# Optimization experiments

Hardware: AMD Instinct MI355X
Metric: run time of the kernel (lower is better)

The kernel has to match this reference:

```python
import jax, jax.numpy as jnp
import numpy as np

B, E, H, T = 32768, 64, 128, 12  # batch, embedding_dim, decoder_h_dim, pred_len


def setup_inputs() -> dict:
    key = jax.random.key(0)
    ks = jax.random.split(key, 13)
    f = lambda k, shape: jax.random.normal(k, shape, dtype=jnp.float32) * 0.05
    return {
        "last_pos": f(ks[0], (B, 2)),
        "last_pos_rel": f(ks[1], (B, 2)),
        "h0": f(ks[2], (1, B, H)),
        "c0": f(ks[3], (1, B, H)),
        "pred_ped_speed": jax.random.uniform(ks[4], (T, B, 1), dtype=jnp.float32),
        # spatial_embedding: Linear(3, E)
        "W_se": f(ks[5], (E, 3)),
        "b_se": f(ks[6], (E,)),
        # single-layer LSTM(E -> H), torch gate order [i, f, g, o]
        "W_ih": f(ks[7], (4 * H, E)),
        "W_hh": f(ks[8], (4 * H, H)),
        "b_ih": f(ks[9], (4 * H,)),
        "b_hh": f(ks[10], (4 * H,)),
        # hidden2pos: Linear(H, 2)
        "W_hp": f(ks[11], (2, H)),
        "b_hp": f(ks[12], (2,)),
    }


def reference(last_pos, last_pos_rel, h0, c0, pred_ped_speed,
              W_se, b_se, W_ih, W_hh, b_ih, b_hh, W_hp, b_hp):
    # train_or_test == 0 path: speed comes straight from pred_ped_speed
    Tlen = pred_ped_speed.shape[0]
    b_lstm = b_ih + b_hh
    # initial decoder input: embed concat([last_pos_rel, speed_0])  -> [B, E]
    x0 = jnp.concatenate([last_pos_rel, pred_ped_speed[0]], axis=1) @ W_se.T + b_se

    def step(carry, t):
        h, c, x, lp = carry  # h,c: [B,H]; x: [B,E]; lp: [B,2]
        gates = x @ W_ih.T + h @ W_hh.T + b_lstm           # [B, 4H]
        i, f_, g, o = jnp.split(gates, 4, axis=1)
        c = jax.nn.sigmoid(f_) * c + jax.nn.sigmoid(i) * jnp.tanh(g)
        h = jax.nn.sigmoid(o) * jnp.tanh(c)
        rel = h @ W_hp.T + b_hp                            # [B, 2]
        lp = rel + lp                                      # curr_pos -> last_pos
        # speed for next step; at final step torch keeps the previous speed
        spd = pred_ped_speed[jnp.minimum(t + 1, Tlen - 1)]
        x = jnp.concatenate([rel, spd], axis=1) @ W_se.T + b_se
        return (h, c, x, lp), rel

    (h, c, _, _), rels = jax.lax.scan(
        step, (h0[0], c0[0], x0, last_pos), jnp.arange(Tlen))
    # pred_traj_fake_rel: [T, B, 2]; final hidden state: [1, B, H]
    return rels, h[None]
```

## Files before the change

kernel.cpp:

```cpp
#include <hip/hip_runtime.h>

#define T_LEN 12
#define B_N   32768
#define H_N   128
#define E_N   64
#define BM    32

typedef __attribute__((ext_vector_type(8))) __bf16 bf16x8;
typedef __attribute__((ext_vector_type(8))) short  short8v;
typedef __attribute__((ext_vector_type(4))) float  f32x4;

__device__ __forceinline__ unsigned short f2bf(float f) {
  unsigned int u = __builtin_bit_cast(unsigned int, f);
  u += 0x7fffu + ((u >> 16) & 1u);
  return (unsigned short)(u >> 16);
}
__device__ __forceinline__ float sigm(float x) {
  return __builtin_amdgcn_rcpf(1.f + __builtin_amdgcn_exp2f(-1.4426950408889634f * x));
}
__device__ __forceinline__ float tanh_(float x) {
  return 1.f - 2.f * __builtin_amdgcn_rcpf(__builtin_amdgcn_exp2f(2.8853900817779268f * x) + 1.f);
}

__global__ void prep_kernel(const float* __restrict__ Wih, const float* __restrict__ Whh,
                            const float* __restrict__ bih, const float* __restrict__ bhh,
                            const float* __restrict__ Wse, const float* __restrict__ bse,
                            const float* __restrict__ Whp, const float* __restrict__ bhp,
                            unsigned short* __restrict__ Wf, float* __restrict__ u,
                            float* __restrict__ w0, float* __restrict__ G) {
  int i = blockIdx.x * 256 + threadIdx.x;
  if (i < 512 * 128) {
    int n = i >> 7, k = i & 127;
    float s = Whh[n * 128 + k];
    float wh0 = Whp[k], wh1 = Whp[128 + k];
    for (int e = 0; e < 64; ++e)
      s += Wih[n * 64 + e] * (Wse[e * 3 + 0] * wh0 + Wse[e * 3 + 1] * wh1);
    Wf[i] = f2bf(s);
  } else if (i < 512 * 128 + 2048) {
    int j = i - 512 * 128;
    int n = j >> 2, which = j & 3;
    float s = 0.f;
    if (which < 2) {
      for (int e = 0; e < 64; ++e) s += Wih[n * 64 + e] * Wse[e * 3 + which];
      G[n * 2 + which] = s;
    } else if (which == 2) {
      for (int e = 0; e < 64; ++e) s += Wih[n * 64 + e] * Wse[e * 3 + 2];
      u[n] = s;
    } else {
      for (int e = 0; e < 64; ++e)
        s += Wih[n * 64 + e] * (bse[e] + Wse[e * 3 + 0] * bhp[0] + Wse[e * 3 + 1] * bhp[1]);
      w0[n] = bih[n] + bhh[n] + s;
    }
  }
}

__launch_bounds__(512, 4)
__global__ void decoder_kernel(const float* __restrict__ lpr,
                               const float* __restrict__ h0,
                               const float* __restrict__ c0,
                               const float* __restrict__ pps,
                               const float* __restrict__ Whp,
                               const float* __restrict__ bhp,
                               const unsigned short* __restrict__ Wf,
                               const float* __restrict__ u,
                               const float* __restrict__ w0,
                               const float* __restrict__ G,
                               float* __restrict__ out_rel,
                               float* __restrict__ out_h) {
  __shared__ unsigned short WfL[256 * 128];
  __shared__ unsigned short hS[BM * 128];
  __shared__ unsigned short whpB[4 * 64 * 8];
  __shared__ float spdbuf[BM];
  __shared__ float dbuf[BM * 2];

  const int tid  = threadIdx.x;
  const int w    = tid >> 6;
  const int l    = tid & 63;
  const int l15  = l & 15;
  const int lg   = l >> 4;
  const int brow = blockIdx.x * BM;
  const int nh   = w * 16 + l15;
  const int swz  = (l15 & 7) << 4;
  char* hB  = (char*)hS;
  char* wB  = (char*)WfL;
  char* pB  = (char*)whpB;

  for (int i = tid; i < 256 * 16; i += 512) {
    int row = i >> 4, k16 = i & 15;
    short8v v = *(const short8v*)(Wf + (256 + row) * 128 + k16 * 8);
    int byte = (row * 256 + k16 * 16) ^ ((row & 7) << 4);
    *(short8v*)(wB + byte) = v;
  }
  short8v bw[2][4];
#pragma unroll
  for (int g = 0; g < 2; ++g)
#pragma unroll
    for (int ks = 0; ks < 4; ++ks)
      bw[g][ks] = *(const short8v*)(Wf + (g * 128 + nh) * 128 + ks * 32 + lg * 8);

  float ur[4], w0r[4];
#pragma unroll
  for (int g = 0; g < 4; ++g) { ur[g] = u[g * 128 + nh]; w0r[g] = w0[g * 128 + nh]; }

  f32x4 cst[2];
#pragma unroll
  for (int mt = 0; mt < 2; ++mt)
#pragma unroll
    for (int r = 0; r < 4; ++r)
      cst[mt][r] = c0[(brow + mt * 16 + lg * 4 + r) * H_N + nh];

  {
    int row = tid >> 4, k0 = (tid & 15) * 8;
    const float* src = h0 + (brow + row) * H_N + k0;
    unsigned short tmp[8];
#pragma unroll
    for (int j = 0; j < 8; ++j) tmp[j] = f2bf(src[j]);
    int byte = (row * 256 + k0 * 2) ^ ((row & 7) << 4);
    *(short8v*)(hB + byte) = *(short8v*)tmp;
  }
  if (tid < 256) {
    int ks = tid >> 6, ll = tid & 63, c = ll & 15, kg = ll >> 4;
    unsigned short tmp[8];
#pragma unroll
    for (int j = 0; j < 8; ++j)
      tmp[j] = (c < 2) ? f2bf(Whp[c * 128 + ks * 32 + kg * 8 + j]) : (unsigned short)0;
    *(short8v*)(pB + (ks * 64 + ll) * 16) = *(short8v*)tmp;
  }
  {
    int dot = tid >> 3, part = tid & 7;
    int row = dot >> 1, j = dot & 1;
    float s = 0.f;
    const float* hrow = h0 + (brow + row) * H_N + part * 16;
    const float* wrow = Whp + j * 128 + part * 16;
#pragma unroll
    for (int k = 0; k < 16; ++k) s += hrow[k] * wrow[k];
    s += __shfl_xor(s, 1); s += __shfl_xor(s, 2); s += __shfl_xor(s, 4);
    if (part == 0) dbuf[dot] = lpr[(brow + row) * 2 + j] - bhp[j] - s;
  }
  const float bhpr = (l15 < 2) ? bhp[l15] : 0.f;

#pragma unroll 1
  for (int t = 0; t < T_LEN; ++t) {
    __syncthreads();

    if (tid < BM) spdbuf[tid] = pps[t * B_N + brow + tid];

    f32x4 acc[4][2];
#pragma unroll
    for (int g = 0; g < 4; ++g)
#pragma unroll
      for (int mt = 0; mt < 2; ++mt) acc[g][mt] = (f32x4){0.f, 0.f, 0.f, 0.f};
    f32x4 relC = (f32x4){0.f, 0.f, 0.f, 0.f};

#pragma unroll
    for (int ks = 0; ks < 4; ++ks) {
      int kb = ks * 64 + lg * 16;
      bf16x8 a0 = __builtin_bit_cast(bf16x8, *(short8v*)(hB + ((l15 * 256 + kb) ^ swz)));
      bf16x8 a1 = __builtin_bit_cast(bf16x8, *(short8v*)(hB + (((16 + l15) * 256 + kb) ^ swz)));
      bf16x8 b2 = __builtin_bit_cast(bf16x8, *(short8v*)(wB + ((nh * 256 + kb) ^ swz)));
      bf16x8 b3 = __builtin_bit_cast(bf16x8, *(short8v*)(wB + 32768 + ((nh * 256 + kb) ^ swz)));
      acc[0][0] = __builtin_amdgcn_mfma_f32_16x16x32_bf16(a0, __builtin_bit_cast(bf16x8, bw[0][ks]), acc[0][0], 0, 0, 0);
      acc[0][1] = __builtin_amdgcn_mfma_f32_16x16x32_bf16(a1, __builtin_bit_cast(bf16x8, bw[0][ks]), acc[0][1], 0, 0, 0);
      acc[1][0] = __builtin_amdgcn_mfma_f32_16x16x32_bf16(a0, __builtin_bit_cast(bf16x8, bw[1][ks]), acc[1][0], 0, 0, 0);
      acc[1][1] = __builtin_amdgcn_mfma_f32_16x16x32_bf16(a1, __builtin_bit_cast(bf16x8, bw[1][ks]), acc[1][1], 0, 0, 0);
      acc[2][0] = __builtin_amdgcn_mfma_f32_16x16x32_bf16(a0, b2, acc[2][0], 0, 0, 0);
      acc[2][1] = __builtin_amdgcn_mfma_f32_16x16x32_bf16(a1, b2, acc[2][1], 0, 0, 0);
      acc[3][0] = __builtin_amdgcn_mfma_f32_16x16x32_bf16(a0, b3, acc[3][0], 0, 0, 0);
      acc[3][1] = __builtin_amdgcn_mfma_f32_16x16x32_bf16(a1, b3, acc[3][1], 0, 0, 0);
      if (w < 2 && t > 0) {
        bf16x8 wb = __builtin_bit_cast(bf16x8, *(short8v*)(pB + ks * 1024 + l * 16));
        relC = __builtin_amdgcn_mfma_f32_16x16x32_bf16(w == 0 ? a0 : a1, wb, relC, 0, 0, 0);
      }
    }
    if (w < 2 && t > 0 && l15 < 2) {
#pragma unroll
      for (int r = 0; r < 4; ++r)
        out_rel[(size_t)(t - 1) * B_N * 2 + (brow + w * 16 + lg * 4 + r) * 2 + l15] = relC[r] + bhpr;
    }

    __syncthreads();

#pragma unroll
    for (int mt = 0; mt < 2; ++mt) {
#pragma unroll
      for (int r = 0; r < 4; ++r) {
        int row = mt * 16 + lg * 4 + r;
        float spd = spdbuf[row];
        float gi = acc[0][mt][r] + w0r[0] + spd * ur[0];
        float gf = acc[1][mt][r] + w0r[1] + spd * ur[1];
        float gg = acc[2][mt][r] + w0r[2] + spd * ur[2];
        float go = acc[3][mt][r] + w0r[3] + spd * ur[3];
        if (t == 0) {
          float d0 = dbuf[row * 2 + 0], d1 = dbuf[row * 2 + 1];
          gi += d0 * G[(0 * 128 + nh) * 2 + 0] + d1 * G[(0 * 128 + nh) * 2 + 1];
          gf += d0 * G[(1 * 128 + nh) * 2 + 0] + d1 * G[(1 * 128 + nh) * 2 + 1];
          gg += d0 * G[(2 * 128 + nh) * 2 + 0] + d1 * G[(2 * 128 + nh) * 2 + 1];
          go += d0 * G[(3 * 128 + nh) * 2 + 0] + d1 * G[(3 * 128 + nh) * 2 + 1];
        }
        float cn = sigm(gf) * cst[mt][r] + sigm(gi) * tanh_(gg);
        cst[mt][r] = cn;
        float h = sigm(go) * tanh_(cn);
        hS[((row * 256 + nh * 2) ^ ((row & 7) << 4)) >> 1] = f2bf(h);
        if (t == T_LEN - 1) out_h[(brow + row) * H_N + nh] = h;
      }
    }
  }

  __syncthreads();
  if (w < 2) {
    f32x4 relC = (f32x4){0.f, 0.f, 0.f, 0.f};
#pragma unroll
    for (int ks = 0; ks < 4; ++ks) {
      int kb = ks * 64 + lg * 16;
      bf16x8 a = __builtin_bit_cast(bf16x8,
          *(short8v*)(hB + (((w * 16 + l15) * 256 + kb) ^ swz)));
      bf16x8 wb = __builtin_bit_cast(bf16x8, *(short8v*)(pB + ks * 1024 + l * 16));
      relC = __builtin_amdgcn_mfma_f32_16x16x32_bf16(a, wb, relC, 0, 0, 0);
    }
    if (l15 < 2) {
#pragma unroll
      for (int r = 0; r < 4; ++r)
        out_rel[(size_t)(T_LEN - 1) * B_N * 2 + (brow + w * 16 + lg * 4 + r) * 2 + l15] = relC[r] + bhpr;
    }
  }
}

extern "C" void kernel_launch(void* const* d_in, const int* in_sizes, int n_in,
                              void* d_out, int out_size, void* d_ws, size_t ws_size,
                              hipStream_t stream) {
  const float* lpr  = (const float*)d_in[1];
  const float* h0   = (const float*)d_in[2];
  const float* c0   = (const float*)d_in[3];
  const float* pps  = (const float*)d_in[4];
  const float* W_se = (const float*)d_in[5];
  const float* b_se = (const float*)d_in[6];
  const float* W_ih = (const float*)d_in[7];
  const float* W_hh = (const float*)d_in[8];
  const float* b_ih = (const float*)d_in[9];
  const float* b_hh = (const float*)d_in[10];
  const float* W_hp = (const float*)d_in[11];
  const float* b_hp = (const float*)d_in[12];

  unsigned short* Wf = (unsigned short*)d_ws;
  float* u  = (float*)((char*)d_ws + 131072);
  float* w0 = (float*)((char*)d_ws + 133120);
  float* G  = (float*)((char*)d_ws + 135168);

  float* out_rel = (float*)d_out;
  float* out_h   = out_rel + (size_t)T_LEN * B_N * 2;

  hipLaunchKernelGGL(prep_kernel, dim3((512 * 128 + 2048 + 255) / 256), dim3(256), 0, stream,
                     W_ih, W_hh, b_ih, b_hh, W_se, b_se, W_hp, b_hp, Wf, u, w0, G);
  hipLaunchKernelGGL(decoder_kernel, dim3(B_N / BM), dim3(512), 0, stream,
                     lpr, h0, c0, pps, W_hp, b_hp, Wf, u, w0, G, out_rel, out_h);
}
```

Baseline: 261.8 us.

## Double-buffer hidden state, keep three gates in registers, prelayout weights in prep

The hidden-state buffer in shared memory is now double-buffered, which removes the second barrier per timestep. The gate MFMAs are split by row tile so the elementwise LSTM update follows each tile's MFMAs directly. Weights for three gates stay in registers, and only the o-gate and hidden2pos weights sit in shared memory. The prep kernel now writes weights in fragment-ready layouts, and speeds, G and biases are preloaded once, with bias folded into the accumulator init. This raises register pressure (48 more VGPRs of weights) and could hurt occupancy under launch_bounds(512,4).

```diff
diff --git a/kernel.cpp b/kernel.cpp
--- a/kernel.cpp
+++ b/kernel.cpp
@@ -3,7 +3,6 @@
 #define T_LEN 12
 #define B_N   32768
 #define H_N   128
-#define E_N   64
 #define BM    32
 
 typedef __attribute__((ext_vector_type(8))) __bf16 bf16x8;
@@ -26,18 +25,23 @@
                             const float* __restrict__ bih, const float* __restrict__ bhh,
                             const float* __restrict__ Wse, const float* __restrict__ bse,
                             const float* __restrict__ Whp, const float* __restrict__ bhp,
-                            unsigned short* __restrict__ Wf, float* __restrict__ u,
+                            unsigned short* __restrict__ WfReg, unsigned short* __restrict__ WfO,
+                            unsigned short* __restrict__ pBg, float* __restrict__ u,
                             float* __restrict__ w0, float* __restrict__ G) {
   int i = blockIdx.x * 256 + threadIdx.x;
-  if (i < 512 * 128) {
-    int n = i >> 7, k = i & 127;
-    float s = Whh[n * 128 + k];
+  if (i < 65536) {
+    int row = i >> 7, k = i & 127;
+    float s = Whh[row * 128 + k];
     float wh0 = Whp[k], wh1 = Whp[128 + k];
     for (int e = 0; e < 64; ++e)
-      s += Wih[n * 64 + e] * (Wse[e * 3 + 0] * wh0 + Wse[e * 3 + 1] * wh1);
-    Wf[i] = f2bf(s);
-  } else if (i < 512 * 128 + 2048) {
-    int j = i - 512 * 128;
+      s += Wih[row * 64 + e] * (Wse[e * 3 + 0] * wh0 + Wse[e * 3 + 1] * wh1);
+    unsigned short v = f2bf(s);
+    int g = row >> 7, unit = row & 127, w = unit >> 4, l15 = unit & 15;
+    int ks = k >> 5, kg = (k >> 3) & 3, j = k & 7, l = kg * 16 + l15;
+    if (g < 3) WfReg[((g * 4 + ks) * 512 + w * 64 + l) * 8 + j] = v;
+    else       WfO[(ks * 512 + w * 64 + l) * 8 + j] = v;
+  } else if (i < 65536 + 2048) {
+    int j = i - 65536;
     int n = j >> 2, which = j & 3;
     float s = 0.f;
     if (which < 2) {
@@ -51,6 +55,11 @@
         s += Wih[n * 64 + e] * (bse[e] + Wse[e * 3 + 0] * bhp[0] + Wse[e * 3 + 1] * bhp[1]);
       w0[n] = bih[n] + bhh[n] + s;
     }
+  } else if (i < 65536 + 2048 + 2048) {
+    int idx = i - 65536 - 2048;
+    int ks = idx >> 9, l = (idx >> 3) & 63, j = idx & 7;
+    int c = l & 15, kg = l >> 4;
+    pBg[idx] = (c < 2) ? f2bf(Whp[c * 128 + ks * 32 + kg * 8 + j]) : (unsigned short)0;
   }
 }
 
@@ -61,17 +70,20 @@
                                const float* __restrict__ pps,
                                const float* __restrict__ Whp,
                                const float* __restrict__ bhp,
-                               const unsigned short* __restrict__ Wf,
+                               const unsigned short* __restrict__ WfReg,
+                               const unsigned short* __restrict__ WfO,
+                               const unsigned short* __restrict__ pBg,
                                const float* __restrict__ u,
                                const float* __restrict__ w0,
                                const float* __restrict__ G,
                                float* __restrict__ out_rel,
                                float* __restrict__ out_h) {
-  __shared__ unsigned short WfL[256 * 128];
-  __shared__ unsigned short hS[BM * 128];
-  __shared__ unsigned short whpB[4 * 64 * 8];
-  __shared__ float spdbuf[BM];
+  __shared__ unsigned short hA[2][BM * 128];
+  __shared__ unsigned short WoL[16384];
+  __shared__ unsigned short pBL[2048];
+  __shared__ float spdL[T_LEN * BM];
   __shared__ float dbuf[BM * 2];
+  __shared__ float GL[1024];
 
   const int tid  = threadIdx.x;
   const int w    = tid >> 6;
@@ -80,34 +92,33 @@
   const int lg   = l >> 4;
   const int brow = blockIdx.x * BM;
   const int nh   = w * 16 + l15;
-  const int swz  = (l15 & 7) << 4;
-  char* hB  = (char*)hS;
-  char* wB  = (char*)WfL;
-  char* pB  = (char*)whpB;
-
-  for (int i = tid; i < 256 * 16; i += 512) {
-    int row = i >> 4, k16 = i & 15;
-    short8v v = *(const short8v*)(Wf + (256 + row) * 128 + k16 * 8);
-    int byte = (row * 256 + k16 * 16) ^ ((row & 7) << 4);
-    *(short8v*)(wB + byte) = v;
-  }
-  short8v bw[2][4];
-#pragma unroll
-  for (int g = 0; g < 2; ++g)
+  const int swzA = (l15 & 7) << 4;
+
+  short8v bw[3][4];
+#pragma unroll
+  for (int g = 0; g < 3; ++g)
 #pragma unroll
     for (int ks = 0; ks < 4; ++ks)
-      bw[g][ks] = *(const short8v*)(Wf + (g * 128 + nh) * 128 + ks * 32 + lg * 8);
-
-  float ur[4], w0r[4];
-#pragma unroll
-  for (int g = 0; g < 4; ++g) { ur[g] = u[g * 128 + nh]; w0r[g] = w0[g * 128 + nh]; }
+      bw[g][ks] = *(const short8v*)(WfReg + ((g * 4 + ks) * 512 + tid) * 8);
+#pragma unroll
+  for (int it = 0; it < 4; ++it) {
+    int idx = it * 512 + tid;
+    *(short8v*)(WoL + idx * 8) = *(const short8v*)(WfO + idx * 8);
+  }
+  if (tid < 256) *(short8v*)(pBL + tid * 8) = *(const short8v*)(pBg + tid * 8);
+  for (int i = tid; i < 1024; i += 512) GL[i] = G[i];
+  if (tid < T_LEN * BM) spdL[tid] = pps[(tid >> 5) * B_N + brow + (tid & 31)];
+
+  float w0r[4], ur[4];
+#pragma unroll
+  for (int g = 0; g < 4; ++g) { w0r[g] = w0[g * 128 + nh]; ur[g] = u[g * 128 + nh]; }
 
   f32x4 cst[2];
 #pragma unroll
-  for (int mt = 0; mt < 2; ++mt)
+  for (int rt = 0; rt < 2; ++rt)
 #pragma unroll
     for (int r = 0; r < 4; ++r)
-      cst[mt][r] = c0[(brow + mt * 16 + lg * 4 + r) * H_N + nh];
+      cst[rt][r] = c0[(brow + rt * 16 + lg * 4 + r) * H_N + nh];
 
   {
     int row = tid >> 4, k0 = (tid & 15) * 8;
@@ -115,61 +126,72 @@
     unsigned short tmp[8];
 #pragma unroll
     for (int j = 0; j < 8; ++j) tmp[j] = f2bf(src[j]);
-    int byte = (row * 256 + k0 * 2) ^ ((row & 7) << 4);
-    *(short8v*)(hB + byte) = *(short8v*)tmp;
-  }
-  if (tid < 256) {
-    int ks = tid >> 6, ll = tid & 63, c = ll & 15, kg = ll >> 4;
-    unsigned short tmp[8];
-#pragma unroll
-    for (int j = 0; j < 8; ++j)
-      tmp[j] = (c < 2) ? f2bf(Whp[c * 128 + ks * 32 + kg * 8 + j]) : (unsigned short)0;
-    *(short8v*)(pB + (ks * 64 + ll) * 16) = *(short8v*)tmp;
+    *(short8v*)((char*)&hA[0][0] + ((row * 256 + k0 * 2) ^ ((row & 7) << 4))) = *(short8v*)tmp;
   }
   {
     int dot = tid >> 3, part = tid & 7;
-    int row = dot >> 1, j = dot & 1;
+    int row = dot >> 1, jj = dot & 1;
     float s = 0.f;
     const float* hrow = h0 + (brow + row) * H_N + part * 16;
-    const float* wrow = Whp + j * 128 + part * 16;
+    const float* wrow = Whp + jj * 128 + part * 16;
 #pragma unroll
     for (int k = 0; k < 16; ++k) s += hrow[k] * wrow[k];
     s += __shfl_xor(s, 1); s += __shfl_xor(s, 2); s += __shfl_xor(s, 4);
-    if (part == 0) dbuf[dot] = lpr[(brow + row) * 2 + j] - bhp[j] - s;
+    if (part == 0) dbuf[dot] = lpr[(brow + row) * 2 + jj] - bhp[jj] - s;
   }
   const float bhpr = (l15 < 2) ? bhp[l15] : 0.f;
+
+  char* rb = (char*)&hA[0][0];
+  char* wbuf = (char*)&hA[1][0];
 
 #pragma unroll 1
   for (int t = 0; t < T_LEN; ++t) {
     __syncthreads();
-
-    if (tid < BM) spdbuf[tid] = pps[t * B_N + brow + tid];
-
-    f32x4 acc[4][2];
-#pragma unroll
-    for (int g = 0; g < 4; ++g)
-#pragma unroll
-      for (int mt = 0; mt < 2; ++mt) acc[g][mt] = (f32x4){0.f, 0.f, 0.f, 0.f};
     f32x4 relC = (f32x4){0.f, 0.f, 0.f, 0.f};
 
 #pragma unroll
-    for (int ks = 0; ks < 4; ++ks) {
-      int kb = ks * 64 + lg * 16;
-      bf16x8 a0 = __builtin_bit_cast(bf16x8, *(short8v*)(hB + ((l15 * 256 + kb) ^ swz)));
-      bf16x8 a1 = __builtin_bit_cast(bf16x8, *(short8v*)(hB + (((16 + l15) * 256 + kb) ^ swz)));
-      bf16x8 b2 = __builtin_bit_cast(bf16x8, *(short8v*)(wB + ((nh * 256 + kb) ^ swz)));
-      bf16x8 b3 = __builtin_bit_cast(bf16x8, *(short8v*)(wB + 32768 + ((nh * 256 + kb) ^ swz)));
-      acc[0][0] = __builtin_amdgcn_mfma_f32_16x16x32_bf16(a0, __builtin_bit_cast(bf16x8, bw[0][ks]), acc[0][0], 0, 0, 0);
-      acc[0][1] = __builtin_amdgcn_mfma_f32_16x16x32_bf16(a1, __builtin_bit_cast(bf16x8, bw[0][ks]), acc[0][1], 0, 0, 0);
-      acc[1][0] = __builtin_amdgcn_mfma_f32_16x16x32_bf16(a0, __builtin_bit_cast(bf16x8, bw[1][ks]), acc[1][0], 0, 0, 0);
-      acc[1][1] = __builtin_amdgcn_mfma_f32_16x16x32_bf16(a1, __builtin_bit_cast(bf16x8, bw[1][ks]), acc[1][1], 0, 0, 0);
-      acc[2][0] = __builtin_amdgcn_mfma_f32_16x16x32_bf16(a0, b2, acc[2][0], 0, 0, 0);
-      acc[2][1] = __builtin_amdgcn_mfma_f32_16x16x32_bf16(a1, b2, acc[2][1], 0, 0, 0);
-      acc[3][0] = __builtin_amdgcn_mfma_f32_16x16x32_bf16(a0, b3, acc[3][0], 0, 0, 0);
-      acc[3][1] = __builtin_amdgcn_mfma_f32_16x16x32_bf16(a1, b3, acc[3][1], 0, 0, 0);
-      if (w < 2 && t > 0) {
-        bf16x8 wb = __builtin_bit_cast(bf16x8, *(short8v*)(pB + ks * 1024 + l * 16));
-        relC = __builtin_amdgcn_mfma_f32_16x16x32_bf16(w == 0 ? a0 : a1, wb, relC, 0, 0, 0);
+    for (int rt = 0; rt < 2; ++rt) {
+      f32x4 acc[4];
+#pragma unroll
+      for (int g = 0; g < 4; ++g) acc[g] = (f32x4){w0r[g], w0r[g], w0r[g], w0r[g]};
+
+#pragma unroll
+      for (int ks = 0; ks < 4; ++ks) {
+        bf16x8 a = __builtin_bit_cast(bf16x8,
+            *(short8v*)(rb + (((rt * 16 + l15) * 256 + ks * 64 + lg * 16) ^ swzA)));
+        bf16x8 bo = __builtin_bit_cast(bf16x8, *(short8v*)(WoL + (ks * 512 + l + w * 64) * 8));
+        acc[0] = __builtin_amdgcn_mfma_f32_16x16x32_bf16(a, __builtin_bit_cast(bf16x8, bw[0][ks]), acc[0], 0, 0, 0);
+        acc[1] = __builtin_amdgcn_mfma_f32_16x16x32_bf16(a, __builtin_bit_cast(bf16x8, bw[1][ks]), acc[1], 0, 0, 0);
+        acc[2] = __builtin_amdgcn_mfma_f32_16x16x32_bf16(a, __builtin_bit_cast(bf16x8, bw[2][ks]), acc[2], 0, 0, 0);
+        acc[3] = __builtin_amdgcn_mfma_f32_16x16x32_bf16(a, bo, acc[3], 0, 0, 0);
+        if (w == rt && t > 0) {
+          bf16x8 pb = __builtin_bit_cast(bf16x8, *(short8v*)(pBL + (ks * 64 + l) * 8));
+          relC = __builtin_amdgcn_mfma_f32_16x16x32_bf16(a, pb, relC, 0, 0, 0);
+        }
+      }
+      if (t == 0) {
+#pragma unroll
+        for (int r = 0; r < 4; ++r) {
+          int row = rt * 16 + lg * 4 + r;
+          float d0 = dbuf[row * 2 + 0], d1 = dbuf[row * 2 + 1];
+#pragma unroll
+          for (int g = 0; g < 4; ++g)
+            acc[g][r] += d0 * GL[(g * 128 + nh) * 2 + 0] + d1 * GL[(g * 128 + nh) * 2 + 1];
+        }
+      }
+#pragma unroll
+      for (int r = 0; r < 4; ++r) {
+        int row = rt * 16 + lg * 4 + r;
+        float spd = spdL[t * BM + row];
+        float gi = __builtin_fmaf(spd, ur[0], acc[0][r]);
+        float gf = __builtin_fmaf(spd, ur[1], acc[1][r]);
+        float gg = __builtin_fmaf(spd, ur[2], acc[2][r]);
+        float go = __builtin_fmaf(spd, ur[3], acc[3][r]);
+        float cn = sigm(gf) * cst[rt][r] + sigm(gi) * tanh_(gg);
+        cst[rt][r] = cn;
+        float h = sigm(go) * tanh_(cn);
+        *(unsigned short*)(wbuf + ((row * 256 + nh * 2) ^ ((row & 7) << 4))) = f2bf(h);
+        if (t == T_LEN - 1) out_h[(brow + row) * H_N + nh] = h;
       }
     }
     if (w < 2 && t > 0 && l15 < 2) {
@@ -177,33 +199,7 @@
       for (int r = 0; r < 4; ++r)
         out_rel[(size_t)(t - 1) * B_N * 2 + (brow + w * 16 + lg * 4 + r) * 2 + l15] = relC[r] + bhpr;
     }
-
-    __syncthreads();
-
-#pragma unroll
-    for (int mt = 0; mt < 2; ++mt) {
-#pragma unroll
-      for (int r = 0; r < 4; ++r) {
-        int row = mt * 16 + lg * 4 + r;
-        float spd = spdbuf[row];
-        float gi = acc[0][mt][r] + w0r[0] + spd * ur[0];
-        float gf = acc[1][mt][r] + w0r[1] + spd * ur[1];
-        float gg = acc[2][mt][r] + w0r[2] + spd * ur[2];
-        float go = acc[3][mt][r] + w0r[3] + spd * ur[3];
-        if (t == 0) {
-          float d0 = dbuf[row * 2 + 0], d1 = dbuf[row * 2 + 1];
-          gi += d0 * G[(0 * 128 + nh) * 2 + 0] + d1 * G[(0 * 128 + nh) * 2 + 1];
-          gf += d0 * G[(1 * 128 + nh) * 2 + 0] + d1 * G[(1 * 128 + nh) * 2 + 1];
-          gg += d0 * G[(2 * 128 + nh) * 2 + 0] + d1 * G[(2 * 128 + nh) * 2 + 1];
-          go += d0 * G[(3 * 128 + nh) * 2 + 0] + d1 * G[(3 * 128 + nh) * 2 + 1];
-        }
-        float cn = sigm(gf) * cst[mt][r] + sigm(gi) * tanh_(gg);
-        cst[mt][r] = cn;
-        float h = sigm(go) * tanh_(cn);
-        hS[((row * 256 + nh * 2) ^ ((row & 7) << 4)) >> 1] = f2bf(h);
-        if (t == T_LEN - 1) out_h[(brow + row) * H_N + nh] = h;
-      }
-    }
+    char* tmpp = rb; rb = wbuf; wbuf = tmpp;
   }
 
   __syncthreads();
@@ -211,11 +207,10 @@
     f32x4 relC = (f32x4){0.f, 0.f, 0.f, 0.f};
 #pragma unroll
     for (int ks = 0; ks < 4; ++ks) {
-      int kb = ks * 64 + lg * 16;
       bf16x8 a = __builtin_bit_cast(bf16x8,
-          *(short8v*)(hB + (((w * 16 + l15) * 256 + kb) ^ swz)));
-      bf16x8 wb = __builtin_bit_cast(bf16x8, *(short8v*)(pB + ks * 1024 + l * 16));
-      relC = __builtin_amdgcn_mfma_f32_16x16x32_bf16(a, wb, relC, 0, 0, 0);
+          *(short8v*)(rb + (((w * 16 + l15) * 256 + ks * 64 + lg * 16) ^ swzA)));
+      bf16x8 pb = __builtin_bit_cast(bf16x8, *(short8v*)(pBL + (ks * 64 + l) * 8));
+      relC = __builtin_amdgcn_mfma_f32_16x16x32_bf16(a, pb, relC, 0, 0, 0);
     }
     if (l15 < 2) {
 #pragma unroll
@@ -241,16 +236,20 @@
   const float* W_hp = (const float*)d_in[11];
   const float* b_hp = (const float*)d_in[12];
 
-  unsigned short* Wf = (unsigned short*)d_ws;
-  float* u  = (float*)((char*)d_ws + 131072);
-  float* w0 = (float*)((char*)d_ws + 133120);
-  float* G  = (float*)((char*)d_ws + 135168);
+  unsigned short* WfReg = (unsigned short*)d_ws;
+  unsigned short* WfO   = (unsigned short*)((char*)d_ws + 98304);
+  unsigned short* pBg   = (unsigned short*)((char*)d_ws + 131072);
+  float* u  = (float*)((char*)d_ws + 135168);
+  float* w0 = (float*)((char*)d_ws + 137216);
+  float* G  = (float*)((char*)d_ws + 139264);
 
   float* out_rel = (float*)d_out;
   float* out_h   = out_rel + (size_t)T_LEN * B_N * 2;
 
-  hipLaunchKernelGGL(prep_kernel, dim3((512 * 128 + 2048 + 255) / 256), dim3(256), 0, stream,
-                     W_ih, W_hh, b_ih, b_hh, W_se, b_se, W_hp, b_hp, Wf, u, w0, G);
+  hipLaunchKernelGGL(prep_kernel, dim3((65536 + 4096 + 255) / 256), dim3(256), 0, stream,
+                     W_ih, W_hh, b_ih, b_hh, W_se, b_se, W_hp, b_hp,
+                     WfReg, WfO, pBg, u, w0, G);
   hipLaunchKernelGGL(decoder_kernel, dim3(B_N / BM), dim3(512), 0, stream,
-                     lpr, h0, c0, pps, W_hp, b_hp, Wf, u, w0, G, out_rel, out_h);
-}
+                     lpr, h0, c0, pps, W_hp, b_hp, WfReg, WfO, pBg, u, w0, G,
+                     out_rel, out_h);
+}
```

After: 274.6 us. 4.9% more time.
